# Performance work log

Hardware: AMD Instinct MI355X
Metric: run time of the kernel (lower is better)

The kernel has to match this reference:

```python
import jax, jax.numpy as jnp
import numpy as np

N = 100000   # nodes
E = 400000   # edges
R = 237      # relations
D = 200      # feature dim (dims=[200,200,200])
B = 4096     # triple batch
L = 2        # num GAT layers
ALPHA = 0.01 # leaky-relu slope


def setup_inputs() -> dict:
    key = jax.random.key(0)
    ks = jax.random.split(key, 11)
    return dict(
        ent_embed=jax.random.normal(ks[0], (N, D), jnp.float32),
        rel_embed=jax.random.normal(ks[1], (R, D), jnp.float32),
        W_gat=jax.random.normal(ks[2], (L, D, D), jnp.float32) * 0.1,
        att_a=jax.random.normal(ks[3], (L, 2 * D), jnp.float32) * 0.1,
        W_hw=jax.random.normal(ks[4], (D, D), jnp.float32) * 0.1,
        b_hw=jax.random.normal(ks[5], (1, D), jnp.float32) * 0.1,
        edge_src=jax.random.randint(ks[6], (E,), 0, N),
        edge_dst=jax.random.randint(ks[7], (E,), 0, N),
        batch_h=jax.random.randint(ks[8], (B,), 0, N),
        batch_r=jax.random.randint(ks[9], (B,), 0, R),
        batch_t=jax.random.randint(ks[10], (B,), 0, N),
    )


def _gat_layer(x, W, a, src, dst):
    # x: [N,D], W: [D,D], a: [2D]
    Wh = x @ W                                  # [N,D]
    s_src = Wh @ a[:D]                          # [N] source score
    s_dst = Wh @ a[D:]                          # [N] dest score
    e = jax.nn.leaky_relu(s_src[src] + s_dst[dst], ALPHA)  # [E]
    # segment softmax over incoming edges of each destination node
    m = jax.ops.segment_max(e, dst, num_segments=N)
    m = jax.lax.stop_gradient(jnp.where(jnp.isfinite(m), m, 0.0))
    ex = jnp.exp(e - m[dst])
    denom = jax.ops.segment_sum(ex, dst, num_segments=N)
    att = ex / jnp.maximum(denom[dst], 1e-9)    # [E]
    out = jax.ops.segment_sum(att[:, None] * Wh[src], dst, num_segments=N)  # [N,D]
    return jax.nn.sigmoid(out)                  # act = torch.sigmoid, 1 head, concat=False


def reference(ent_embed, rel_embed, W_gat, att_a, W_hw, b_hw,
              edge_src, edge_dst, batch_h, batch_r, batch_t):
    x = ent_embed
    for i in range(L):
        gat_out = _gat_layer(x, W_gat[i], att_a[i], edge_src, edge_dst)
        # highway gate: sigma = sigmoid(x W + b); shared W,b across layers
        sigma = jax.nn.sigmoid(x @ W_hw + b_hw)
        x = sigma * gat_out + (1.0 - sigma) * x
    h = x[batch_h]
    r = rel_embed[batch_r]
    t = x[batch_t]
    return (h, r, t)
```

## Files before the change

### kernel.cpp

```cpp
#include <hip/hip_runtime.h>
#include <math.h>

#define NNODES 100000
#define NEDGES 400000
#define DIM    200
#define NB     4096
#define NL     2
#define ALPHA  0.01f
#define D4     (DIM/4)
#define NPAD   100096
#define KPAD   224
#define NKS    7
#define NCF    26
#define NBB    (2*NB)
#define NBLK   ((NNODES + 255) / 256)
#define SCAN_BPB 1024
#define NSB    ((NNODES + SCAN_BPB - 1) / SCAN_BPB)
#define GFULL  (NPAD / 32)
#define CSBLK  ((NPAD * 32) / 256)
#define HBLK   ((NEDGES + 255) / 256)
#define PREPBLK ((2 * NKS * NCF * 64 + NL * 2 * DIM + 255) / 256)
#define SGB    (NBB / 32)
#define RELB   ((NB * D4 + 447) / 448)

typedef __attribute__((ext_vector_type(8))) short short8;
typedef __attribute__((ext_vector_type(4))) float f32x4;

__device__ __forceinline__ float sigm(float v) { return 1.0f / (1.0f + expf(-v)); }
__device__ __forceinline__ unsigned short f2bf(float f) {
    unsigned u = __float_as_uint(f);
    unsigned r = u + 0x7fff + ((u >> 16) & 1);
    return (unsigned short)(r >> 16);
}
__device__ __forceinline__ float bflo(unsigned u) { return __uint_as_float(u << 16); }
__device__ __forceinline__ float bfhi(unsigned u) { return __uint_as_float(u & 0xffff0000u); }

template<int MODE>
__global__ __launch_bounds__(256) void scanlb_k(const int* __restrict__ in,
                                                int* __restrict__ state,
                                                int* __restrict__ ticket,
                                                int* __restrict__ o0,
                                                int* __restrict__ o1,
                                                int* __restrict__ o2)
{
    __shared__ int sbid;
    __shared__ int tmp[256];
    __shared__ int sexcl;
    int tid = threadIdx.x;
    if (tid == 0) sbid = atomicAdd(ticket, 1);
    __syncthreads();
    int bid = sbid;
    int base = bid * SCAN_BPB + tid * 4;

    int4 v4 = make_int4(0, 0, 0, 0);
    if (base + 3 < NNODES) v4 = *(const int4*)(in + base);
    else {
        if (base + 0 < NNODES) v4.x = in[base + 0];
        if (base + 1 < NNODES) v4.y = in[base + 1];
        if (base + 2 < NNODES) v4.z = in[base + 2];
    }
    int s1 = v4.x + v4.y, s2 = s1 + v4.z, s3 = s2 + v4.w;

    tmp[tid] = s3; __syncthreads();
#pragma unroll
    for (int off = 1; off < 256; off <<= 1) {
        int t = (tid >= off) ? tmp[tid - off] : 0;
        __syncthreads();
        tmp[tid] += t;
        __syncthreads();
    }
    int bexcl_t = tmp[tid] - s3;
    int btotal  = tmp[255];

    if (tid == 0) {
        int st = (bid == 0) ? ((2 << 30) | btotal) : ((1 << 30) | btotal);
        __hip_atomic_store(&state[bid], st, __ATOMIC_RELEASE, __HIP_MEMORY_SCOPE_AGENT);
        if (bid == 0) sexcl = 0;
    }
    if (bid > 0 && tid < 64) {
        int excl = 0;
        int pred = bid - 1;
        while (pred >= -64) {
            int idx = pred - tid;
            int s = (idx >= 0)
                ? __hip_atomic_load(&state[idx], __ATOMIC_ACQUIRE, __HIP_MEMORY_SCOPE_AGENT)
                : (2 << 30);
            int f = ((unsigned)s) >> 30;
            unsigned long long nv = __ballot(f == 0);
            unsigned long long iv = __ballot(f == 2);
            int firstnv = nv ? (__ffsll(nv) - 1) : 64;
            int firstiv = iv ? (__ffsll(iv) - 1) : 64;
            if (firstiv < firstnv) {
                int contrib = (tid <= firstiv) ? (s & 0x3FFFFFFF) : 0;
#pragma unroll
                for (int m = 32; m; m >>= 1) contrib += __shfl_xor(contrib, m, 64);
                excl += contrib;
                break;
            } else if (firstnv > 0) {
                int contrib = (tid < firstnv) ? (s & 0x3FFFFFFF) : 0;
#pragma unroll
                for (int m = 32; m; m >>= 1) contrib += __shfl_xor(contrib, m, 64);
                excl += contrib;
                pred -= firstnv;
            }
        }
        if (tid == 0) {
            __hip_atomic_store(&state[bid], (2 << 30) | (excl + btotal),
                               __ATOMIC_RELEASE, __HIP_MEMORY_SCOPE_AGENT);
            sexcl = excl;
        }
    }
    __syncthreads();
    int ex = sexcl + bexcl_t;

    if (MODE == 0) {
        int4 r = make_int4(ex, ex + v4.x, ex + s1, ex + s2);
        if (base + 3 < NNODES) {
            *(int4*)(o0 + base) = r;
            *(int4*)(o1 + base) = r;
        } else {
            if (base + 0 < NNODES) { o0[base + 0] = r.x; o1[base + 0] = r.x; }
            if (base + 1 < NNODES) { o0[base + 1] = r.y; o1[base + 1] = r.y; }
            if (base + 2 < NNODES) { o0[base + 2] = r.z; o1[base + 2] = r.z; }
        }
        if (bid == NSB - 1 && tid == 0) o0[NNODES] = NEDGES;
    } else {
        int vv[4] = { v4.x, v4.y, v4.z, v4.w };
        int ee[4] = { ex, ex + v4.x, ex + s1, ex + s2 };
#pragma unroll
        for (int j = 0; j < 4; ++j) {
            int idx = base + j;
            if (idx < NNODES) {
                if (vv[j]) { o0[ee[j]] = idx; o1[idx] = ee[j]; }
                if (idx == NNODES - 1) *o2 = ee[j] + vv[j];
            }
        }
    }
}

__global__ void scatter_k(const int* __restrict__ src, const int* __restrict__ dst,
                          int* __restrict__ cursor, int* __restrict__ csr_src)
{
    int e = blockIdx.x * blockDim.x + threadIdx.x;
    if (e >= NEDGES) return;
    int d = dst[e];
    int p = atomicAdd(&cursor[d], 1);
    csr_src[p] = src[e];
}

__global__ void mark_k(const int* __restrict__ bh, const int* __restrict__ bt,
                       const int* __restrict__ rs, const int* __restrict__ csr_src,
                       int* __restrict__ mask)
{
    int e = blockIdx.x * 256 + threadIdx.x;
    if (e >= NBB) return;
    int node = (e < NB) ? bh[e] : bt[e - NB];
    mask[node] = 1;
    int b = rs[node], en = rs[node + 1];
    for (int j = b; j < en; ++j) mask[csr_src[j]] = 1;
}

__global__ __launch_bounds__(256) void zeroprep_k(int* __restrict__ deg, int* __restrict__ mask,
                                                  int* __restrict__ lbbuf,
                                                  const float* __restrict__ Wg,
                                                  const float* __restrict__ Whw,
                                                  const float* __restrict__ aa,
                                                  unsigned short* __restrict__ wp0,
                                                  unsigned short* __restrict__ wp1,
                                                  float* __restrict__ wv)
{
    int bid = blockIdx.x, tid = threadIdx.x;
    if (bid < NBLK) {
        int i = bid * 256 + tid;
        if (i < NNODES) { deg[i] = 0; mask[i] = 0; }
        if (i < 320) lbbuf[i] = 0;
        return;
    }
    int t0 = (bid - NBLK) * 256 + tid;
    const int WP = NKS * NCF * 64;
    if (t0 < 2 * WP) {
        int pk = (t0 >= WP) ? 1 : 0;
        int t = t0 - pk * WP;
        const float* Wgl = Wg + (size_t)pk * DIM * DIM;
        unsigned short* wp = pk ? wp1 : wp0;
        int l = t & 63, cf = (t >> 6) % NCF, ks = t / (NCF * 64);
        int col = (cf % 13) * 16 + (l & 15);
        const float* W = (cf < 13) ? Wgl : Whw;
        unsigned rr[4];
#pragma unroll
        for (int j = 0; j < 4; ++j) {
            int ka = ks * 32 + (l >> 4) * 8 + 2 * j;
            float fa = (ka < DIM && col < DIM) ? W[ka * DIM + col] : 0.f;
            float fb = (ka + 1 < DIM && col < DIM) ? W[(ka + 1) * DIM + col] : 0.f;
            rr[j] = (unsigned)f2bf(fa) | ((unsigned)f2bf(fb) << 16);
        }
        ((uint4*)wp)[t] = make_uint4(rr[0], rr[1], rr[2], rr[3]);
    } else {
        int u = t0 - 2 * WP;
        if (u >= NL * 2 * DIM) return;
        int l = u / (2 * DIM), sd = (u / DIM) % 2, k = u % DIM;
        const float* W = Wg + (size_t)l * DIM * DIM + (size_t)k * DIM;
        const float* av = aa + (size_t)l * 2 * DIM + sd * DIM;
        float s = 0.f;
        for (int c = 0; c < DIM; ++c) s = fmaf(W[c], av[c], s);
        wv[u] = s;
    }
}

__global__ __launch_bounds__(256) void convscorehist_k(const float* __restrict__ xin,
                                                       const float* __restrict__ wvl,
                                                       unsigned short* __restrict__ ap,
                                                       float* __restrict__ s_src,
                                                       float* __restrict__ s_dst,
                                                       const int* __restrict__ edst,
                                                       int* __restrict__ deg)
{
    int bid = blockIdx.x, tid = threadIdx.x;
    if (bid < HBLK) {
        int e = bid * 256 + tid;
        if (e < NEDGES) atomicAdd(&deg[edst[e]], 1);
        return;
    }
    int gt = (bid - HBLK) * 256 + tid;
    int row = gt >> 5, hl = gt & 31;

    float ps = 0.f, pd = 0.f;
    if (hl < 28) {
        uint4 o = make_uint4(0u, 0u, 0u, 0u);
        if (row < NNODES && hl < 25) {
            size_t base = (size_t)row * D4 + hl * 2;
            float4 x0 = ((const float4*)xin)[base];
            float4 x1 = ((const float4*)xin)[base + 1];
            o.x = (unsigned)f2bf(x0.x) | ((unsigned)f2bf(x0.y) << 16);
            o.y = (unsigned)f2bf(x0.z) | ((unsigned)f2bf(x0.w) << 16);
            o.z = (unsigned)f2bf(x1.x) | ((unsigned)f2bf(x1.y) << 16);
            o.w = (unsigned)f2bf(x1.z) | ((unsigned)f2bf(x1.w) << 16);
            float4 s0 = ((const float4*)wvl)[hl * 2];
            float4 s1 = ((const float4*)wvl)[hl * 2 + 1];
            float4 d0 = ((const float4*)(wvl + DIM))[hl * 2];
            float4 d1 = ((const float4*)(wvl + DIM))[hl * 2 + 1];
            ps = x0.x*s0.x + x0.y*s0.y + x0.z*s0.z + x0.w*s0.w
               + x1.x*s1.x + x1.y*s1.y + x1.z*s1.z + x1.w*s1.w;
            pd = x0.x*d0.x + x0.y*d0.y + x0.z*d0.z + x0.w*d0.w
               + x1.x*d1.x + x1.y*d1.y + x1.z*d1.z + x1.w*d1.w;
        }
        ((uint4*)ap)[(size_t)row * 28 + hl] = o;
    }
#pragma unroll
    for (int m = 16; m; m >>= 1) {
        ps += __shfl_xor(ps, m, 32);
        pd += __shfl_xor(pd, m, 32);
    }
    if (hl == 0 && row < NNODES) { s_src[row] = ps; s_dst[row] = pd; }
}

template<int CFBASE, int IND>
__device__ __forceinline__ void gemm_body(const unsigned short* __restrict__ Apack,
                                          const unsigned short* __restrict__ Wpack,
                                          const float* __restrict__ bhw,
                                          unsigned short* __restrict__ outb,
                                          const int* __restrict__ Lrow,
                                          const int* __restrict__ bh,
                                          const int* __restrict__ bt,
                                          int nrows, int vb, int tid)
{
    int rowbase = vb * 32;
    if (rowbase >= nrows) return;

    int w = tid >> 6;
    int l = tid & 63;
    int cgrp = l >> 4, cidx = l & 15;
    int cf0 = CFBASE + 2 * w;
    int cf1 = CFBASE + 2 * w + 1;
    int cf1l = (cf1 < NCF) ? cf1 : (NCF - 1);

    const short8* Bp = (const short8*)Wpack + l;
    short8 b0[NKS], b1[NKS];
#pragma unroll
    for (int ks = 0; ks < NKS; ++ks) {
        b0[ks] = Bp[(ks * NCF + cf0) * 64];
        b1[ks] = Bp[(ks * NCF + cf1l) * 64];
    }

    int e0 = rowbase + cidx, e1 = rowbase + 16 + cidx;
    int ar0, ar1;
    if (IND == 1) {
        ar0 = Lrow[min(e0, nrows - 1)];
        ar1 = Lrow[min(e1, nrows - 1)];
    } else if (IND == 2) {
        int c0 = min(e0, nrows - 1), c1 = min(e1, nrows - 1);
        ar0 = (c0 < NB) ? bh[c0] : bt[c0 - NB];
        ar1 = (c1 < NB) ? bh[c1] : bt[c1 - NB];
    } else { ar0 = e0; ar1 = e1; }

    const short8* Ap0 = (const short8*)(Apack + (size_t)ar0 * KPAD + cgrp * 8);
    const short8* Ap1 = (const short8*)(Apack + (size_t)ar1 * KPAD + cgrp * 8);

    f32x4 acc00 = (f32x4){0.f,0.f,0.f,0.f}, acc01 = acc00, acc10 = acc00, acc11 = acc00;

    short8 a0[2], a1[2];
    a0[0] = Ap0[0];
    a1[0] = Ap1[0];

#pragma unroll
    for (int ks = 0; ks < NKS; ++ks) {
        const int cur = ks & 1, nxt = cur ^ 1;
        if (ks + 1 < NKS) {
            a0[nxt] = Ap0[(ks + 1) * 4];
            a1[nxt] = Ap1[(ks + 1) * 4];
        }
        acc00 = __builtin_amdgcn_mfma_f32_16x16x32_bf16(a0[cur], b0[ks], acc00, 0, 0, 0);
        acc01 = __builtin_amdgcn_mfma_f32_16x16x32_bf16(a0[cur], b1[ks], acc01, 0, 0, 0);
        acc10 = __builtin_amdgcn_mfma_f32_16x16x32_bf16(a1[cur], b0[ks], acc10, 0, 0, 0);
        acc11 = __builtin_amdgcn_mfma_f32_16x16x32_bf16(a1[cur], b1[ks], acc11, 0, 0, 0);
    }

#pragma unroll
    for (int cc = 0; cc < 2; ++cc) {
        int cf = cc ? cf1 : cf0;
        if (cf >= CFBASE + 13) continue;
        int col = (cf - CFBASE) * 16 + cidx;
        if (col >= DIM) continue;
        f32x4 ar_0 = cc ? acc01 : acc00;
        f32x4 ar_1 = cc ? acc11 : acc10;
        if (CFBASE == 0) {
#pragma unroll
            for (int r = 0; r < 4; ++r) {
                int row = rowbase + cgrp * 4 + r;
                if (row < nrows) outb[(size_t)row * DIM + col] = f2bf(ar_0[r]);
                row += 16;
                if (row < nrows) outb[(size_t)row * DIM + col] = f2bf(ar_1[r]);
            }
        } else {
            float bb2 = bhw[col];
#pragma unroll
            for (int r = 0; r < 4; ++r) {
                int row = rowbase + cgrp * 4 + r;
                if (row < nrows) outb[(size_t)row * DIM + col] = f2bf(sigm(ar_0[r] + bb2));
                row += 16;
                if (row < nrows) outb[(size_t)row * DIM + col] = f2bf(sigm(ar_1[r] + bb2));
            }
        }
    }
}

__global__ __launch_bounds__(448) void gemm_whb_k(const unsigned short* __restrict__ Apack,
                                                  const unsigned short* __restrict__ Wpack,
                                                  unsigned short* __restrict__ whb)
{
    gemm_body<0, 0>(Apack, Wpack, nullptr, whb, nullptr, nullptr, nullptr,
                    NNODES, blockIdx.x, threadIdx.x);
}

__global__ __launch_bounds__(448) void gemm_sgc_k(const unsigned short* __restrict__ Apack,
                                                  const unsigned short* __restrict__ Wpack,
                                                  const float* __restrict__ bhw,
                                                  unsigned short* __restrict__ sgc,
                                                  const int* __restrict__ Lrow,
                                                  const int* __restrict__ nLp)
{
    gemm_body<13, 1>(Apack, Wpack, bhw, sgc, Lrow, nullptr, nullptr,
                     *nLp, blockIdx.x, threadIdx.x);
}

__global__ __launch_bounds__(256) void agg3c_k(const int* __restrict__ csr_src,
                                               const int* __restrict__ rs,
                                               const float* __restrict__ s_src,
                                               const float* __restrict__ s_dst,
                                               const unsigned short* __restrict__ whb,
                                               const unsigned short* __restrict__ sgc,
                                               unsigned short* __restrict__ apack,
                                               const int* __restrict__ Lrow,
                                               const int* __restrict__ nLp,
                                               const float* __restrict__ wvn,
                                               float* __restrict__ o_ssrc,
                                               float* __restrict__ o_sdst)
{
    int gt = blockIdx.x * 256 + threadIdx.x;
    int lidx = gt >> 5;
    int hl = gt & 31;
    if (lidx >= *nLp) return;
    int node = Lrow[lidx];

    int beg = rs[node], end = rs[node + 1];
    float sd = s_dst[node];

    float m = -3.4e38f;
    for (int j = beg + hl; j < end; j += 32) {
        float v = s_src[csr_src[j]] + sd;
        v = v > 0.f ? v : ALPHA * v;
        m = fmaxf(m, v);
    }
#pragma unroll
    for (int s = 16; s; s >>= 1) m = fmaxf(m, __shfl_xor(m, s, 32));
    float sum = 0.f;
    for (int j = beg + hl; j < end; j += 32) {
        float v = s_src[csr_src[j]] + sd;
        v = v > 0.f ? v : ALPHA * v;
        sum += expf(v - m);
    }
#pragma unroll
    for (int s = 16; s; s >>= 1) sum += __shfl_xor(sum, s, 32);
    float inv_ = 1.f / fmaxf(sum, 1e-9f);

    float ps = 0.f, pd = 0.f;
    if (hl < 25) {
        float av[8] = {0.f, 0.f, 0.f, 0.f, 0.f, 0.f, 0.f, 0.f};
        int j = beg;
        for (; j + 1 < end; j += 2) {
            int n0 = csr_src[j], n1 = csr_src[j + 1];
            float v0 = s_src[n0] + sd, v1 = s_src[n1] + sd;
            v0 = v0 > 0.f ? v0 : ALPHA * v0;
            v1 = v1 > 0.f ? v1 : ALPHA * v1;
            float c0 = expf(v0 - m) * inv_, c1 = expf(v1 - m) * inv_;
            uint4 w0 = ((const uint4*)whb)[(size_t)n0 * 25 + hl];
            uint4 w1 = ((const uint4*)whb)[(size_t)n1 * 25 + hl];
            av[0] = fmaf(c0, bflo(w0.x), av[0]); av[0] = fmaf(c1, bflo(w1.x), av[0]);
            av[1] = fmaf(c0, bfhi(w0.x), av[1]); av[1] = fmaf(c1, bfhi(w1.x), av[1]);
            av[2] = fmaf(c0, bflo(w0.y), av[2]); av[2] = fmaf(c1, bflo(w1.y), av[2]);
            av[3] = fmaf(c0, bfhi(w0.y), av[3]); av[3] = fmaf(c1, bfhi(w1.y), av[3]);
            av[4] = fmaf(c0, bflo(w0.z), av[4]); av[4] = fmaf(c1, bflo(w1.z), av[4]);
            av[5] = fmaf(c0, bfhi(w0.z), av[5]); av[5] = fmaf(c1, bfhi(w1.z), av[5]);
            av[6] = fmaf(c0, bflo(w0.w), av[6]); av[6] = fmaf(c1, bflo(w1.w), av[6]);
            av[7] = fmaf(c0, bfhi(w0.w), av[7]); av[7] = fmaf(c1, bfhi(w1.w), av[7]);
        }
        if (j < end) {
            int n0 = csr_src[j];
            float v0 = s_src[n0] + sd;
            v0 = v0 > 0.f ? v0 : ALPHA * v0;
            float c0 = expf(v0 - m) * inv_;
            uint4 w0 = ((const uint4*)whb)[(size_t)n0 * 25 + hl];
            av[0] = fmaf(c0, bflo(w0.x), av[0]);
            av[1] = fmaf(c0, bfhi(w0.x), av[1]);
            av[2] = fmaf(c0, bflo(w0.y), av[2]);
            av[3] = fmaf(c0, bfhi(w0.y), av[3]);
            av[4] = fmaf(c0, bflo(w0.z), av[4]);
            av[5] = fmaf(c0, bfhi(w0.z), av[5]);
            av[6] = fmaf(c0, bflo(w0.w), av[6]);
            av[7] = fmaf(c0, bfhi(w0.w), av[7]);
        }

        uint4 sv = ((const uint4*)sgc)[(size_t)lidx * 25 + hl];
        uint4 xv = ((const uint4*)apack)[(size_t)node * 28 + hl];
        float4 o0, o1;
        float s0;
        s0 = bflo(sv.x); o0.x = s0 * sigm(av[0]) + (1.f - s0) * bflo(xv.x);
        s0 = bfhi(sv.x); o0.y = s0 * sigm(av[1]) + (1.f - s0) * bfhi(xv.x);
        s0 = bflo(sv.y); o0.z = s0 * sigm(av[2]) + (1.f - s0) * bflo(xv.y);
        s0 = bfhi(sv.y); o0.w = s0 * sigm(av[3]) + (1.f - s0) * bfhi(xv.y);
        s0 = bflo(sv.z); o1.x = s0 * sigm(av[4]) + (1.f - s0) * bflo(xv.z);
        s0 = bfhi(sv.z); o1.y = s0 * sigm(av[5]) + (1.f - s0) * bfhi(xv.z);
        s0 = bflo(sv.w); o1.z = s0 * sigm(av[6]) + (1.f - s0) * bflo(xv.w);
        s0 = bfhi(sv.w); o1.w = s0 * sigm(av[7]) + (1.f - s0) * bfhi(xv.w);

        unsigned r0 = (unsigned)f2bf(o0.x) | ((unsigned)f2bf(o0.y) << 16);
        unsigned r1 = (unsigned)f2bf(o0.z) | ((unsigned)f2bf(o0.w) << 16);
        unsigned r2 = (unsigned)f2bf(o1.x) | ((unsigned)f2bf(o1.y) << 16);
        unsigned r3 = (unsigned)f2bf(o1.z) | ((unsigned)f2bf(o1.w) << 16);
        ((uint4*)apack)[(size_t)node * 28 + hl] = make_uint4(r0, r1, r2, r3);

        float4 ws0 = ((const float4*)wvn)[hl * 2];
        float4 ws1 = ((const float4*)wvn)[hl * 2 + 1];
        float4 wd0 = ((const float4*)(wvn + DIM))[hl * 2];
        float4 wd1 = ((const float4*)(wvn + DIM))[hl * 2 + 1];
        ps = o0.x*ws0.x + o0.y*ws0.y + o0.z*ws0.z + o0.w*ws0.w
           + o1.x*ws1.x + o1.y*ws1.y + o1.z*ws1.z + o1.w*ws1.w;
        pd = o0.x*wd0.x + o0.y*wd0.y + o0.z*wd0.z + o0.w*wd0.w
           + o1.x*wd1.x + o1.y*wd1.y + o1.z*wd1.z + o1.w*wd1.w;
    }
#pragma unroll
    for (int s = 16; s; s >>= 1) {
        ps += __shfl_xor(ps, s, 32);
        pd += __shfl_xor(pd, s, 32);
    }
    if (hl == 0) { o_ssrc[node] = ps; o_sdst[node] = pd; }
}

__global__ __launch_bounds__(448) void l1pack_k(const unsigned short* __restrict__ Apack,
                                                const unsigned short* __restrict__ Wpack1,
                                                const float* __restrict__ bhw,
                                                unsigned short* __restrict__ whc,
                                                unsigned short* __restrict__ sgbatch,
                                                const int* __restrict__ Lrow,
                                                const int* __restrict__ nLp,
                                                const int* __restrict__ bh,
                                                const int* __restrict__ bt,
                                                const float* __restrict__ rel,
                                                const int* __restrict__ br,
                                                float* __restrict__ out)
{
    int bid = blockIdx.x, tid = threadIdx.x;
    if (bid < GFULL) {
        gemm_body<0, 1>(Apack, Wpack1, bhw, whc, Lrow, nullptr, nullptr, *nLp, bid, tid);
    } else if (bid < GFULL + SGB) {
        gemm_body<13, 2>(Apack, Wpack1, bhw, sgbatch, nullptr, bh, bt, NBB, bid - GFULL, tid);
    } else {
        int u = (bid - GFULL - SGB) * 448 + tid;
        if (u < NB * D4) {
            int row = u / D4, c = u - row * D4;
            ((float4*)out)[(size_t)(NB + row) * D4 + c] =
                ((const float4*)rel)[(size_t)br[row] * D4 + c];
        }
    }
}

__global__ __launch_bounds__(256) void agg4_k(const int* __restrict__ csr_src,
                                              const int* __restrict__ rs,
                                              const float* __restrict__ s_src,
                                              const float* __restrict__ s_dst,
                                              const unsigned short* __restrict__ whc,
                                              const int* __restrict__ inv,
                                              const unsigned short* __restrict__ sgbatch,
                                              const unsigned short* __restrict__ apack,
                                              const int* __restrict__ bh,
                                              const int* __restrict__ bt,
                                              float* __restrict__ out)
{
    int gt = blockIdx.x * 256 + threadIdx.x;
    int e = gt >> 5;
    int hl = gt & 31;
    if (e >= NBB) return;
    int node = (e < NB) ? bh[e] : bt[e - NB];
    int orow = (e < NB) ? e : (2 * NB + (e - NB));

    int beg = rs[node], end = rs[node + 1];
    float sd = s_dst[node];

    float m = -3.4e38f;
    for (int j = beg + hl; j < end; j += 32) {
        float v = s_src[csr_src[j]] + sd;
        v = v > 0.f ? v : ALPHA * v;
        m = fmaxf(m, v);
    }
#pragma unroll
    for (int s = 16; s; s >>= 1) m = fmaxf(m, __shfl_xor(m, s, 32));
    float sum = 0.f;
    for (int j = beg + hl; j < end; j += 32) {
        float v = s_src[csr_src[j]] + sd;
        v = v > 0.f ? v : ALPHA * v;
        sum += expf(v - m);
    }
#pragma unroll
    for (int s = 16; s; s >>= 1) sum += __shfl_xor(sum, s, 32);
    float inv_ = 1.f / fmaxf(sum, 1e-9f);

    if (hl < 25) {
        float av[8] = {0.f, 0.f, 0.f, 0.f, 0.f, 0.f, 0.f, 0.f};
        int j = beg;
        for (; j + 1 < end; j += 2) {
            int n0 = csr_src[j], n1 = csr_src[j + 1];
            float v0 = s_src[n0] + sd, v1 = s_src[n1] + sd;
            v0 = v0 > 0.f ? v0 : ALPHA * v0;
            v1 = v1 > 0.f ? v1 : ALPHA * v1;
            float c0 = expf(v0 - m) * inv_, c1 = expf(v1 - m) * inv_;
            uint4 w0 = ((const uint4*)whc)[(size_t)inv[n0] * 25 + hl];
            uint4 w1 = ((const uint4*)whc)[(size_t)inv[n1] * 25 + hl];
            av[0] = fmaf(c0, bflo(w0.x), av[0]); av[0] = fmaf(c1, bflo(w1.x), av[0]);
            av[1] = fmaf(c0, bfhi(w0.x), av[1]); av[1] = fmaf(c1, bfhi(w1.x), av[1]);
            av[2] = fmaf(c0, bflo(w0.y), av[2]); av[2] = fmaf(c1, bflo(w1.y), av[2]);
            av[3] = fmaf(c0, bfhi(w0.y), av[3]); av[3] = fmaf(c1, bfhi(w1.y), av[3]);
            av[4] = fmaf(c0, bflo(w0.z), av[4]); av[4] = fmaf(c1, bflo(w1.z), av[4]);
            av[5] = fmaf(c0, bfhi(w0.z), av[5]); av[5] = fmaf(c1, bfhi(w1.z), av[5]);
            av[6] = fmaf(c0, bflo(w0.w), av[6]); av[6] = fmaf(c1, bflo(w1.w), av[6]);
            av[7] = fmaf(c0, bfhi(w0.w), av[7]); av[7] = fmaf(c1, bfhi(w1.w), av[7]);
        }
        if (j < end) {
            int n0 = csr_src[j];
            float v0 = s_src[n0] + sd;
            v0 = v0 > 0.f ? v0 : ALPHA * v0;
            float c0 = expf(v0 - m) * inv_;
            uint4 w0 = ((const uint4*)whc)[(size_t)inv[n0] * 25 + hl];
            av[0] = fmaf(c0, bflo(w0.x), av[0]);
            av[1] = fmaf(c0, bfhi(w0.x), av[1]);
            av[2] = fmaf(c0, bflo(w0.y), av[2]);
            av[3] = fmaf(c0, bfhi(w0.y), av[3]);
            av[4] = fmaf(c0, bflo(w0.z), av[4]);
            av[5] = fmaf(c0, bfhi(w0.z), av[5]);
            av[6] = fmaf(c0, bflo(w0.w), av[6]);
            av[7] = fmaf(c0, bfhi(w0.w), av[7]);
        }

        uint4 sv = ((const uint4*)sgbatch)[(size_t)e * 25 + hl];
        uint4 xv = ((const uint4*)apack)[(size_t)node * 28 + hl];
        float4 o0, o1;
        float s0;
        s0 = bflo(sv.x); o0.x = s0 * sigm(av[0]) + (1.f - s0) * bflo(xv.x);
        s0 = bfhi(sv.x); o0.y = s0 * sigm(av[1]) + (1.f - s0) * bfhi(xv.x);
        s0 = bflo(sv.y); o0.z = s0 * sigm(av[2]) + (1.f - s0) * bflo(xv.y);
        s0 = bfhi(sv.y); o0.w = s0 * sigm(av[3]) + (1.f - s0) * bfhi(xv.y);
        s0 = bflo(sv.z); o1.x = s0 * sigm(av[4]) + (1.f - s0) * bflo(xv.z);
        s0 = bfhi(sv.z); o1.y = s0 * sigm(av[5]) + (1.f - s0) * bfhi(xv.z);
        s0 = bflo(sv.w); o1.z = s0 * sigm(av[6]) + (1.f - s0) * bflo(xv.w);
        s0 = bfhi(sv.w); o1.w = s0 * sigm(av[7]) + (1.f - s0) * bfhi(xv.w);

        size_t base = (size_t)orow * D4 + hl * 2;
        ((float4*)out)[base]     = o0;
        ((float4*)out)[base + 1] = o1;
    }
}

extern "C" void kernel_launch(void* const* d_in, const int* in_sizes, int n_in,
                              void* d_out, int out_size, void* d_ws, size_t ws_size,
                              hipStream_t stream)
{
    const float* ent = (const float*)d_in[0];
    const float* rel = (const float*)d_in[1];
    const float* Wg  = (const float*)d_in[2];
    const float* aa  = (const float*)d_in[3];
    const float* Whw = (const float*)d_in[4];
    const float* bhw = (const float*)d_in[5];
    const int* esrc  = (const int*)d_in[6];
    const int* edst  = (const int*)d_in[7];
    const int* bh    = (const int*)d_in[8];
    const int* br    = (const int*)d_in[9];
    const int* bt    = (const int*)d_in[10];
    float* out = (float*)d_out;

    char* p = (char*)d_ws;
    auto carve = [&](size_t bytes) { char* r = p; p += (bytes + 63) & ~(size_t)63; return r; };
    unsigned short* whb     = (unsigned short*)carve((size_t)NNODES * DIM * 2);
    unsigned short* whc     = (unsigned short*)carve((size_t)NNODES * DIM * 2);
    unsigned short* sgc     = (unsigned short*)carve((size_t)NNODES * DIM * 2);
    unsigned short* apack   = (unsigned short*)carve((size_t)NPAD * KPAD * 2);
    unsigned short* sgbatch = (unsigned short*)carve((size_t)NBB * DIM * 2);
    unsigned short* wp0     = (unsigned short*)carve((size_t)NKS * NCF * 64 * 16);
    unsigned short* wp1     = (unsigned short*)carve((size_t)NKS * NCF * 64 * 16);
    float* wv    = (float*)carve(NL * 2 * DIM * 4);
    float* ss0   = (float*)carve(NNODES * 4);
    float* sd0   = (float*)carve(NNODES * 4);
    float* ss1   = (float*)carve(NNODES * 4);
    float* sd1   = (float*)carve(NNODES * 4);
    int* deg     = (int*)carve(NNODES * 4);
    int* rs      = (int*)carve((NNODES + 1) * 4);
    int* cursor  = (int*)carve(NNODES * 4);
    int* csr_src = (int*)carve(NEDGES * 4);
    int* mask    = (int*)carve(NNODES * 4);
    int* Lrow    = (int*)carve(NNODES * 4);
    int* inv     = (int*)carve(NNODES * 4);
    int* lbbuf   = (int*)carve(320 * 4);
    int* nLp     = (int*)carve(64);

    int* st0   = lbbuf;
    int* st1   = lbbuf + 128;
    int* tick0 = lbbuf + 256;
    int* tick1 = lbbuf + 257;

    zeroprep_k<<<NBLK + PREPBLK, 256, 0, stream>>>(deg, mask, lbbuf,
                                                   Wg, Whw, aa, wp0, wp1, wv);

    convscorehist_k<<<HBLK + CSBLK, 256, 0, stream>>>(ent, wv, apack, ss0, sd0, edst, deg);

    scanlb_k<0><<<NSB, 256, 0, stream>>>(deg, st0, tick0, rs, cursor, nullptr);
    scatter_k<<<(NEDGES + 255) / 256, 256, 0, stream>>>(esrc, edst, cursor, csr_src);
    mark_k<<<(NBB + 255) / 256, 256, 0, stream>>>(bh, bt, rs, csr_src, mask);
    scanlb_k<1><<<NSB, 256, 0, stream>>>(mask, st1, tick1, Lrow, inv, nLp);

    gemm_whb_k<<<GFULL, 448, 0, stream>>>(apack, wp0, whb);
    gemm_sgc_k<<<GFULL, 448, 0, stream>>>(apack, wp0, bhw, sgc, Lrow, nLp);

    agg3c_k<<<(NNODES * 32) / 256, 256, 0, stream>>>(csr_src, rs, ss0, sd0, whb, sgc,
                                                     apack, Lrow, nLp, wv + 2 * DIM, ss1, sd1);

    l1pack_k<<<GFULL + SGB + RELB, 448, 0, stream>>>(apack, wp1, bhw, whc, sgbatch,
                                                     Lrow, nLp, bh, bt, rel, br, out);

    agg4_k<<<(NBB * 32) / 256, 256, 0, stream>>>(csr_src, rs, ss1, sd1, whc, inv,
                                                 sgbatch, apack, bh, bt, out);
}
```

Baseline: 207.9 us.

## Split conversion kernel into slices carried alongside CSR-build and mask phases

The bf16 conversion and score computation, previously fused only with the degree histogram, is cut into five slices. Each slice rides in one of the five serial CSR-construction kernels: histogram, scan, scatter, mark and mask scan. This fills the GPU while those small, latency-bound phases run. The mark phase also changes from one thread per batch node to 32 lanes per node walking the neighbour list in parallel. The risk is that large conversion slices stretch each launch, and that the scan's ticket-based block ordering now runs alongside unrelated blocks.

```diff
diff --git a/kernel.cpp b/kernel.cpp
--- a/kernel.cpp
+++ b/kernel.cpp
@@ -18,7 +18,9 @@
 #define NSB    ((NNODES + SCAN_BPB - 1) / SCAN_BPB)
 #define GFULL  (NPAD / 32)
 #define CSBLK  ((NPAD * 32) / 256)
+#define CONV_SLICE ((CSBLK + 4) / 5)
 #define HBLK   ((NEDGES + 255) / 256)
+#define MARKB  (NBB * 32 / 256)
 #define PREPBLK ((2 * NKS * NCF * 64 + NL * 2 * DIM + 255) / 256)
 #define SGB    (NBB / 32)
 #define RELB   ((NB * D4 + 447) / 448)
@@ -36,17 +38,13 @@
 __device__ __forceinline__ float bfhi(unsigned u) { return __uint_as_float(u & 0xffff0000u); }
 
 template<int MODE>
-__global__ __launch_bounds__(256) void scanlb_k(const int* __restrict__ in,
-                                                int* __restrict__ state,
-                                                int* __restrict__ ticket,
-                                                int* __restrict__ o0,
-                                                int* __restrict__ o1,
-                                                int* __restrict__ o2)
+__device__ void scan_body(const int* __restrict__ in, int* __restrict__ state,
+                          int* __restrict__ ticket, int* __restrict__ o0,
+                          int* __restrict__ o1, int* __restrict__ o2, int tid)
 {
     __shared__ int sbid;
     __shared__ int tmp[256];
     __shared__ int sexcl;
-    int tid = threadIdx.x;
     if (tid == 0) sbid = atomicAdd(ticket, 1);
     __syncthreads();
     int bid = sbid;
@@ -138,91 +136,16 @@
     }
 }
 
-__global__ void scatter_k(const int* __restrict__ src, const int* __restrict__ dst,
-                          int* __restrict__ cursor, int* __restrict__ csr_src)
-{
-    int e = blockIdx.x * blockDim.x + threadIdx.x;
-    if (e >= NEDGES) return;
-    int d = dst[e];
-    int p = atomicAdd(&cursor[d], 1);
-    csr_src[p] = src[e];
-}
-
-__global__ void mark_k(const int* __restrict__ bh, const int* __restrict__ bt,
-                       const int* __restrict__ rs, const int* __restrict__ csr_src,
-                       int* __restrict__ mask)
-{
-    int e = blockIdx.x * 256 + threadIdx.x;
-    if (e >= NBB) return;
-    int node = (e < NB) ? bh[e] : bt[e - NB];
-    mask[node] = 1;
-    int b = rs[node], en = rs[node + 1];
-    for (int j = b; j < en; ++j) mask[csr_src[j]] = 1;
-}
-
-__global__ __launch_bounds__(256) void zeroprep_k(int* __restrict__ deg, int* __restrict__ mask,
-                                                  int* __restrict__ lbbuf,
-                                                  const float* __restrict__ Wg,
-                                                  const float* __restrict__ Whw,
-                                                  const float* __restrict__ aa,
-                                                  unsigned short* __restrict__ wp0,
-                                                  unsigned short* __restrict__ wp1,
-                                                  float* __restrict__ wv)
-{
-    int bid = blockIdx.x, tid = threadIdx.x;
-    if (bid < NBLK) {
-        int i = bid * 256 + tid;
-        if (i < NNODES) { deg[i] = 0; mask[i] = 0; }
-        if (i < 320) lbbuf[i] = 0;
-        return;
-    }
-    int t0 = (bid - NBLK) * 256 + tid;
-    const int WP = NKS * NCF * 64;
-    if (t0 < 2 * WP) {
-        int pk = (t0 >= WP) ? 1 : 0;
-        int t = t0 - pk * WP;
-        const float* Wgl = Wg + (size_t)pk * DIM * DIM;
-        unsigned short* wp = pk ? wp1 : wp0;
-        int l = t & 63, cf = (t >> 6) % NCF, ks = t / (NCF * 64);
-        int col = (cf % 13) * 16 + (l & 15);
-        const float* W = (cf < 13) ? Wgl : Whw;
-        unsigned rr[4];
-#pragma unroll
-        for (int j = 0; j < 4; ++j) {
-            int ka = ks * 32 + (l >> 4) * 8 + 2 * j;
-            float fa = (ka < DIM && col < DIM) ? W[ka * DIM + col] : 0.f;
-            float fb = (ka + 1 < DIM && col < DIM) ? W[(ka + 1) * DIM + col] : 0.f;
-            rr[j] = (unsigned)f2bf(fa) | ((unsigned)f2bf(fb) << 16);
-        }
-        ((uint4*)wp)[t] = make_uint4(rr[0], rr[1], rr[2], rr[3]);
-    } else {
-        int u = t0 - 2 * WP;
-        if (u >= NL * 2 * DIM) return;
-        int l = u / (2 * DIM), sd = (u / DIM) % 2, k = u % DIM;
-        const float* W = Wg + (size_t)l * DIM * DIM + (size_t)k * DIM;
-        const float* av = aa + (size_t)l * 2 * DIM + sd * DIM;
-        float s = 0.f;
-        for (int c = 0; c < DIM; ++c) s = fmaf(W[c], av[c], s);
-        wv[u] = s;
-    }
-}
-
-__global__ __launch_bounds__(256) void convscorehist_k(const float* __restrict__ xin,
-                                                       const float* __restrict__ wvl,
-                                                       unsigned short* __restrict__ ap,
-                                                       float* __restrict__ s_src,
-                                                       float* __restrict__ s_dst,
-                                                       const int* __restrict__ edst,
-                                                       int* __restrict__ deg)
-{
-    int bid = blockIdx.x, tid = threadIdx.x;
-    if (bid < HBLK) {
-        int e = bid * 256 + tid;
-        if (e < NEDGES) atomicAdd(&deg[edst[e]], 1);
-        return;
-    }
-    int gt = (bid - HBLK) * 256 + tid;
+__device__ __forceinline__ void conv_body(const float* __restrict__ xin,
+                                          const float* __restrict__ wvl,
+                                          unsigned short* __restrict__ ap,
+                                          float* __restrict__ s_src,
+                                          float* __restrict__ s_dst,
+                                          int cb, int tid)
+{
+    int gt = cb * 256 + tid;
     int row = gt >> 5, hl = gt & 31;
+    if (row >= NPAD) return;
 
     float ps = 0.f, pd = 0.f;
     if (hl < 28) {
@@ -252,6 +175,97 @@
         pd += __shfl_xor(pd, m, 32);
     }
     if (hl == 0 && row < NNODES) { s_src[row] = ps; s_dst[row] = pd; }
+}
+
+template<int PHASE>
+__global__ __launch_bounds__(256) void carrier_k(
+    const float* __restrict__ xin, const float* __restrict__ wvl,
+    unsigned short* __restrict__ ap, float* __restrict__ ss0, float* __restrict__ sd0,
+    const int* __restrict__ esrc, const int* __restrict__ edst, int* __restrict__ deg,
+    int* __restrict__ st0, int* __restrict__ tick0, int* __restrict__ rs,
+    int* __restrict__ cursor,
+    int* __restrict__ st1, int* __restrict__ tick1, int* __restrict__ Lrow,
+    int* __restrict__ inv, int* __restrict__ nLp,
+    int* __restrict__ csr_src, const int* __restrict__ bh, const int* __restrict__ bt,
+    int* __restrict__ mask, int nsmall)
+{
+    int bid = blockIdx.x, tid = threadIdx.x;
+    if (bid < nsmall) {
+        if (PHASE == 0) {
+            int e = bid * 256 + tid;
+            if (e < NEDGES) atomicAdd(&deg[edst[e]], 1);
+        } else if (PHASE == 1) {
+            scan_body<0>(deg, st0, tick0, rs, cursor, nullptr, tid);
+        } else if (PHASE == 2) {
+            int e = bid * 256 + tid;
+            if (e < NEDGES) {
+                int d = edst[e];
+                int p = atomicAdd(&cursor[d], 1);
+                csr_src[p] = esrc[e];
+            }
+        } else if (PHASE == 3) {
+            int g = bid * 256 + tid;
+            int e = g >> 5, hl = g & 31;
+            if (e < NBB) {
+                int node = (e < NB) ? bh[e] : bt[e - NB];
+                if (hl == 0) mask[node] = 1;
+                int b = rs[node], en = rs[node + 1];
+                for (int j = b + hl; j < en; j += 32) mask[csr_src[j]] = 1;
+            }
+        } else {
+            scan_body<1>(mask, st1, tick1, Lrow, inv, nLp, tid);
+        }
+        return;
+    }
+    int cb = PHASE * CONV_SLICE + (bid - nsmall);
+    if (cb < CSBLK) conv_body(xin, wvl, ap, ss0, sd0, cb, tid);
+}
+
+__global__ __launch_bounds__(256) void zeroprep_k(int* __restrict__ deg, int* __restrict__ mask,
+                                                  int* __restrict__ lbbuf,
+                                                  const float* __restrict__ Wg,
+                                                  const float* __restrict__ Whw,
+                                                  const float* __restrict__ aa,
+                                                  unsigned short* __restrict__ wp0,
+                                                  unsigned short* __restrict__ wp1,
+                                                  float* __restrict__ wv)
+{
+    int bid = blockIdx.x, tid = threadIdx.x;
+    if (bid < NBLK) {
+        int i = bid * 256 + tid;
+        if (i < NNODES) { deg[i] = 0; mask[i] = 0; }
+        if (i < 320) lbbuf[i] = 0;
+        return;
+    }
+    int t0 = (bid - NBLK) * 256 + tid;
+    const int WP = NKS * NCF * 64;
+    if (t0 < 2 * WP) {
+        int pk = (t0 >= WP) ? 1 : 0;
+        int t = t0 - pk * WP;
+        const float* Wgl = Wg + (size_t)pk * DIM * DIM;
+        unsigned short* wp = pk ? wp1 : wp0;
+        int l = t & 63, cf = (t >> 6) % NCF, ks = t / (NCF * 64);
+        int col = (cf % 13) * 16 + (l & 15);
+        const float* W = (cf < 13) ? Wgl : Whw;
+        unsigned rr[4];
+#pragma unroll
+        for (int j = 0; j < 4; ++j) {
+            int ka = ks * 32 + (l >> 4) * 8 + 2 * j;
+            float fa = (ka < DIM && col < DIM) ? W[ka * DIM + col] : 0.f;
+            float fb = (ka + 1 < DIM && col < DIM) ? W[(ka + 1) * DIM + col] : 0.f;
+            rr[j] = (unsigned)f2bf(fa) | ((unsigned)f2bf(fb) << 16);
+        }
+        ((uint4*)wp)[t] = make_uint4(rr[0], rr[1], rr[2], rr[3]);
+    } else {
+        int u = t0 - 2 * WP;
+        if (u >= NL * 2 * DIM) return;
+        int l = u / (2 * DIM), sd = (u / DIM) % 2, k = u % DIM;
+        const float* W = Wg + (size_t)l * DIM * DIM + (size_t)k * DIM;
+        const float* av = aa + (size_t)l * 2 * DIM + sd * DIM;
+        float s = 0.f;
+        for (int c = 0; c < DIM; ++c) s = fmaf(W[c], av[c], s);
+        wv[u] = s;
+    }
 }
 
 template<int CFBASE, int IND>
@@ -648,12 +662,21 @@
     zeroprep_k<<<NBLK + PREPBLK, 256, 0, stream>>>(deg, mask, lbbuf,
                                                    Wg, Whw, aa, wp0, wp1, wv);
 
-    convscorehist_k<<<HBLK + CSBLK, 256, 0, stream>>>(ent, wv, apack, ss0, sd0, edst, deg);
-
-    scanlb_k<0><<<NSB, 256, 0, stream>>>(deg, st0, tick0, rs, cursor, nullptr);
-    scatter_k<<<(NEDGES + 255) / 256, 256, 0, stream>>>(esrc, edst, cursor, csr_src);
-    mark_k<<<(NBB + 255) / 256, 256, 0, stream>>>(bh, bt, rs, csr_src, mask);
-    scanlb_k<1><<<NSB, 256, 0, stream>>>(mask, st1, tick1, Lrow, inv, nLp);
+    carrier_k<0><<<HBLK + CONV_SLICE, 256, 0, stream>>>(ent, wv, apack, ss0, sd0,
+        esrc, edst, deg, st0, tick0, rs, cursor, st1, tick1, Lrow, inv, nLp,
+        csr_src, bh, bt, mask, HBLK);
+    carrier_k<1><<<NSB + CONV_SLICE, 256, 0, stream>>>(ent, wv, apack, ss0, sd0,
+        esrc, edst, deg, st0, tick0, rs, cursor, st1, tick1, Lrow, inv, nLp,
+        csr_src, bh, bt, mask, NSB);
+    carrier_k<2><<<HBLK + CONV_SLICE, 256, 0, stream>>>(ent, wv, apack, ss0, sd0,
+        esrc, edst, deg, st0, tick0, rs, cursor, st1, tick1, Lrow, inv, nLp,
+        csr_src, bh, bt, mask, HBLK);
+    carrier_k<3><<<MARKB + CONV_SLICE, 256, 0, stream>>>(ent, wv, apack, ss0, sd0,
+        esrc, edst, deg, st0, tick0, rs, cursor, st1, tick1, Lrow, inv, nLp,
+        csr_src, bh, bt, mask, MARKB);
+    carrier_k<4><<<NSB + CONV_SLICE, 256, 0, stream>>>(ent, wv, apack, ss0, sd0,
+        esrc, edst, deg, st0, tick0, rs, cursor, st1, tick1, Lrow, inv, nLp,
+        csr_src, bh, bt, mask, NSB);
 
     gemm_whb_k<<<GFULL, 448, 0, stream>>>(apack, wp0, whb);
     gemm_sgc_k<<<GFULL, 448, 0, stream>>>(apack, wp0, bhw, sgc, Lrow, nLp);
```

Measured after the change: 211.2 us. About the same (+1.5%).
